# Kernel tuning notes

Hardware: AMD Instinct MI355X
Metric: run time of the kernel (lower is better)

The kernel has to match this reference:

```python
import jax, jax.numpy as jnp
import numpy as np

DIM = 512
NUM_HEADS = 8
HEAD_DIM = DIM // NUM_HEADS
B, N = 2, 4096


def setup_inputs() -> dict:
    key = jax.random.key(0)
    k1, k2, k3, k4, k5 = jax.random.split(key, 5)
    s = 1.0 / np.sqrt(DIM)
    return {
        "x": jax.random.normal(k1, (B, N, DIM), dtype=jnp.float32),
        "w_qkv": jax.random.normal(k2, (DIM, 3 * DIM), dtype=jnp.float32) * s,
        "b_qkv": jax.random.normal(k3, (3 * DIM,), dtype=jnp.float32) * 0.01,
        "w_proj": jax.random.normal(k4, (DIM, DIM), dtype=jnp.float32) * s,
        "b_proj": jax.random.normal(k5, (DIM,), dtype=jnp.float32) * 0.01,
    }


def reference(x, w_qkv, b_qkv, w_proj, b_proj):
    b, n, c = x.shape
    h, d = NUM_HEADS, HEAD_DIM
    qkv = x @ w_qkv + b_qkv                      # [B,N,3C]
    q, k, v = jnp.split(qkv, 3, axis=-1)
    # [B,N,C] -> [B,H,N,D]
    q = q.reshape(b, n, h, d).transpose(0, 2, 1, 3)
    k = k.reshape(b, n, h, d).transpose(0, 2, 1, 3)
    v = v.reshape(b, n, h, d).transpose(0, 2, 1, 3)
    scale = d ** (-0.5)
    attn = jnp.einsum('bhqd,bhkd->bhqk', q, k) * scale  # [B,H,N,N]
    attn = jax.nn.softmax(attn, axis=-1)
    out = jnp.einsum('bhqk,bhkd->bhqd', attn, v)        # [B,H,N,D]
    out = out.transpose(0, 2, 1, 3).reshape(b, n, c)
    return out @ w_proj + b_proj
```

## Files before the change

kernel.cpp:

```cpp
#include <hip/hip_runtime.h>

#define DIM_C 512
#define HEADS 8
#define HD 64
#define BATCH 2
#define SEQ 4096
#define QSCALE (0.125f * 1.44269504088896f)

typedef __attribute__((ext_vector_type(8))) short short8;
typedef __attribute__((ext_vector_type(4))) float f32x4;

__device__ __forceinline__ ushort f2bf(float f) {
    union { float f; unsigned u; } x; x.f = f;
    unsigned r = x.u + 0x7fffu + ((x.u >> 16) & 1u);
    return (ushort)(r >> 16);
}

__device__ __forceinline__ void gl_lds16(const void* g, void* l) {
    __builtin_amdgcn_global_load_lds(
        (const __attribute__((address_space(1))) unsigned int*)g,
        (__attribute__((address_space(3))) unsigned int*)l, 16, 0, 0);
}

__device__ __forceinline__ unsigned cvt_pk_bf16(float lo, float hi) {
    unsigned w;
    asm("v_cvt_pk_bf16_f32 %0, %1, %2" : "=v"(w) : "v"(lo), "v"(hi));
    return w;
}

__global__ __launch_bounds__(256)
void convert_bf16(const float* __restrict__ in, ushort* __restrict__ out, int n4) {
    int i = blockIdx.x * blockDim.x + threadIdx.x;
    const int stride = gridDim.x * blockDim.x;
    for (; i < n4; i += stride) {
        const float4 v = reinterpret_cast<const float4*>(in)[i];
        ushort4 o;
        o.x = f2bf(v.x); o.y = f2bf(v.y); o.z = f2bf(v.z); o.w = f2bf(v.w);
        reinterpret_cast<ushort4*>(out)[i] = o;
    }
}

__global__ __launch_bounds__(256)
void transpose_w_bf16(const float* __restrict__ in, ushort* __restrict__ out,
                      int R, int C) {
    __shared__ ushort Ls[64 * 68];
    const int tid = threadIdx.x;
    const int c0 = blockIdx.x * 64, r0 = blockIdx.y * 64;
    #pragma unroll
    for (int p = 0; p < 4; ++p) {
        const int idx = tid + p * 256;
        const int r = idx >> 4, c4 = (idx & 15) * 4;
        const float4 v = *reinterpret_cast<const float4*>(
            &in[(size_t)(r0 + r) * C + c0 + c4]);
        ushort4 o; o.x = f2bf(v.x); o.y = f2bf(v.y); o.z = f2bf(v.z); o.w = f2bf(v.w);
        *reinterpret_cast<ushort4*>(&Ls[r * 68 + c4]) = o;
    }
    __syncthreads();
    #pragma unroll
    for (int p = 0; p < 4; ++p) {
        const int idx = tid + p * 256;
        const int c = idx >> 4, r4 = (idx & 15) * 4;
        ushort4 o;
        o.x = Ls[(r4 + 0) * 68 + c]; o.y = Ls[(r4 + 1) * 68 + c];
        o.z = Ls[(r4 + 2) * 68 + c]; o.w = Ls[(r4 + 3) * 68 + c];
        *reinterpret_cast<ushort4*>(&out[(size_t)(c0 + c) * R + r0 + r4]) = o;
    }
}

template<int MODE>
__global__ __launch_bounds__(256)
void gemm_mfma(const ushort* __restrict__ A, const ushort* __restrict__ BT,
               const float* __restrict__ bias, void* __restrict__ Cout,
               ushort* __restrict__ vtOut, int M, int N, int K) {
    __shared__ ushort As[128 * 64];
    __shared__ ushort Bs[128 * 64];
    const int tid = threadIdx.x;
    const int lane = tid & 63, wid = tid >> 6;
    const int lr = lane & 15, lg = lane >> 4;
    const int wm = wid >> 1, wn = wid & 1;
    const int rowBase = blockIdx.y * 128, colBase = blockIdx.x * 128;
    const int l8 = lane >> 3;
    const int lchunk = (lane & 7) ^ l8;

    f32x4 acc[4][4];
    #pragma unroll
    for (int i = 0; i < 4; ++i)
        #pragma unroll
        for (int j = 0; j < 4; ++j)
            #pragma unroll
            for (int c = 0; c < 4; ++c) acc[i][j][c] = 0.f;

    for (int k0 = 0; k0 < K; k0 += 64) {
        #pragma unroll
        for (int i = 0; i < 4; ++i) {
            const int r = wid * 32 + i * 8;
            gl_lds16(&A[(size_t)(rowBase + r + l8) * K + k0 + lchunk * 8],
                     &As[r * 64]);
            gl_lds16(&BT[(size_t)(colBase + r + l8) * K + k0 + lchunk * 8],
                     &Bs[r * 64]);
        }
        __syncthreads();
        #pragma unroll
        for (int s = 0; s < 2; ++s) {
            short8 af[4], bf[4];
            #pragma unroll
            for (int mt = 0; mt < 4; ++mt) {
                const int r = wm * 64 + mt * 16 + lr;
                af[mt] = *reinterpret_cast<const short8*>(
                    &As[r * 64 + ((s * 4 + lg) ^ (r & 7)) * 8]);
            }
            #pragma unroll
            for (int nt = 0; nt < 4; ++nt) {
                const int r = wn * 64 + nt * 16 + lr;
                bf[nt] = *reinterpret_cast<const short8*>(
                    &Bs[r * 64 + ((s * 4 + lg) ^ (r & 7)) * 8]);
            }
            #pragma unroll
            for (int mt = 0; mt < 4; ++mt)
                #pragma unroll
                for (int nt = 0; nt < 4; ++nt)
                    acc[mt][nt] = __builtin_amdgcn_mfma_f32_16x16x32_bf16(
                        af[mt], bf[nt], acc[mt][nt], 0, 0, 0);
        }
        __syncthreads();
    }

    #pragma unroll
    for (int nt = 0; nt < 4; ++nt) {
        const int col = colBase + wn * 64 + nt * 16 + lr;
        const float bv = bias[col];
        if (MODE == 1 && col >= 1024) {
            const int d = col - 1024;
            const int bb = rowBase >> 12;
            const size_t vbase = ((size_t)(bb * 8 + (d >> 6)) * 64 + (d & 63)) * SEQ;
            #pragma unroll
            for (int mt = 0; mt < 4; ++mt) {
                const int n = (rowBase & (SEQ - 1)) + wm * 64 + mt * 16 + lg * 4;
                ushort4 o;
                o.x = f2bf(acc[mt][nt][0] + bv); o.y = f2bf(acc[mt][nt][1] + bv);
                o.z = f2bf(acc[mt][nt][2] + bv); o.w = f2bf(acc[mt][nt][3] + bv);
                *reinterpret_cast<ushort4*>(&vtOut[vbase + n]) = o;
            }
        } else {
            const float qs = (MODE == 1 && col < DIM_C) ? QSCALE : 1.f;
            #pragma unroll
            for (int mt = 0; mt < 4; ++mt) {
                #pragma unroll
                for (int j = 0; j < 4; ++j) {
                    const int row = rowBase + wm * 64 + mt * 16 + lg * 4 + j;
                    const float v = (acc[mt][nt][j] + bv) * qs;
                    if (MODE == 0)
                        reinterpret_cast<float*>(Cout)[(size_t)row * N + col] = v;
                    else
                        reinterpret_cast<ushort*>(Cout)[(size_t)row * N + col] = f2bf(v);
                }
            }
        }
    }
}

__global__ __launch_bounds__(512)
void flash_attn5(const ushort* __restrict__ qkvb, const ushort* __restrict__ vt,
                 ushort* __restrict__ aoutb) {
    __shared__ ushort Ks[2][64 * 64];
    __shared__ ushort Vs[2][64 * 64];
    __shared__ ushort Ps[8 * 16 * 64];

    const int tid = threadIdx.x;
    const int lane = tid & 63, wid = tid >> 6;
    const int lr = lane & 15, lg = lane >> 4;
    const int qt = blockIdx.x, bh = blockIdx.y;
    const int b = bh >> 3, h = bh & 7;
    const int q0 = qt * 128;
    const int l8 = lane >> 3;
    const int lchunk = (lane & 7) ^ l8;

    short8 qf[2];
    {
        const size_t qrow = (size_t)b * SEQ + q0 + wid * 16 + lr;
        #pragma unroll
        for (int s = 0; s < 2; ++s)
            qf[s] = *reinterpret_cast<const short8*>(
                &qkvb[qrow * 1536 + h * 64 + s * 32 + lg * 8]);
    }

    float m = -1e30f, l = 0.f;
    f32x4 oa[4];
    #pragma unroll
    for (int dt = 0; dt < 4; ++dt)
        #pragma unroll
        for (int c = 0; c < 4; ++c) oa[dt][c] = 0.f;

    auto stage = [&](int kt, int buf) {
        const int k0 = kt * 64;
        const int r = wid * 8;
        gl_lds16(&qkvb[(size_t)(b * SEQ + k0 + r + l8) * 1536 + DIM_C +
                       h * 64 + lchunk * 8],
                 &Ks[buf][r * 64]);
        gl_lds16(&vt[((size_t)bh * 64 + r + l8) * SEQ + k0 + lchunk * 8],
                 &Vs[buf][r * 64]);
    };

    stage(0, 0);
    const int NT = SEQ / 64;
    for (int kt = 0; kt < NT; ++kt) {
        const int buf = kt & 1;
        __syncthreads();
        if (kt + 1 < NT) stage(kt + 1, buf ^ 1);

        f32x4 sa[4];
        #pragma unroll
        for (int t = 0; t < 4; ++t)
            #pragma unroll
            for (int c = 0; c < 4; ++c) sa[t][c] = 0.f;
        #pragma unroll
        for (int t = 0; t < 4; ++t) {
            const int n = t * 16 + lr;
            #pragma unroll
            for (int s = 0; s < 2; ++s) {
                const short8 kf = *reinterpret_cast<const short8*>(
                    &Ks[buf][n * 64 + ((s * 4 + lg) ^ (n & 7)) * 8]);
                sa[t] = __builtin_amdgcn_mfma_f32_16x16x32_bf16(
                    kf, qf[s], sa[t], 0, 0, 0);
            }
        }

        float mx = sa[0][0];
        #pragma unroll
        for (int t = 0; t < 4; ++t)
            #pragma unroll
            for (int r = 0; r < 4; ++r) mx = fmaxf(mx, sa[t][r]);
        mx = fmaxf(mx, __shfl_xor(mx, 16));
        mx = fmaxf(mx, __shfl_xor(mx, 32));
        if (__any(mx > m + 8.f)) {
            const float mnew = fmaxf(m, mx);
            const float alpha = exp2f(m - mnew);
            m = mnew;
            l *= alpha;
            const float a0 = __shfl(alpha, lg * 4 + 0);
            const float a1 = __shfl(alpha, lg * 4 + 1);
            const float a2 = __shfl(alpha, lg * 4 + 2);
            const float a3 = __shfl(alpha, lg * 4 + 3);
            #pragma unroll
            for (int dt = 0; dt < 4; ++dt) {
                oa[dt][0] *= a0; oa[dt][1] *= a1;
                oa[dt][2] *= a2; oa[dt][3] *= a3;
            }
        }
        float sum = 0.f;
        #pragma unroll
        for (int t = 0; t < 4; ++t)
            #pragma unroll
            for (int r = 0; r < 4; ++r) {
                sa[t][r] = exp2f(sa[t][r] - m);
                sum += sa[t][r];
            }
        sum += __shfl_xor(sum, 16);
        sum += __shfl_xor(sum, 32);
        l += sum;

        const int pb = wid * (16 * 64);
        const int pbase = pb + lr * 64 + (lg & 1) * 4;
        #pragma unroll
        for (int t = 0; t < 4; ++t) {
            const int chunk = (2 * t + (lg >> 1)) ^ (lr & 7);
            uint2 w;
            w.x = cvt_pk_bf16(sa[t][0], sa[t][1]);
            w.y = cvt_pk_bf16(sa[t][2], sa[t][3]);
            *reinterpret_cast<uint2*>(&Ps[pbase + chunk * 8]) = w;
        }

        short8 pf[2];
        #pragma unroll
        for (int s = 0; s < 2; ++s)
            pf[s] = *reinterpret_cast<const short8*>(
                &Ps[pb + lr * 64 + ((lg * 8 + 32 * s) ^ ((lr & 7) << 3))]);

        #pragma unroll
        for (int dt = 0; dt < 4; ++dt) {
            const int d = dt * 16 + lr;
            #pragma unroll
            for (int s = 0; s < 2; ++s) {
                const short8 vf = *reinterpret_cast<const short8*>(
                    &Vs[buf][d * 64 + ((s * 4 + lg) ^ (d & 7)) * 8]);
                oa[dt] = __builtin_amdgcn_mfma_f32_16x16x32_bf16(
                    pf[s], vf, oa[dt], 0, 0, 0);
            }
        }
    }

    const float linv = 1.f / l;
    const float v0 = __shfl(linv, lg * 4 + 0);
    const float v1 = __shfl(linv, lg * 4 + 1);
    const float v2 = __shfl(linv, lg * 4 + 2);
    const float v3 = __shfl(linv, lg * 4 + 3);
    const size_t orow0 = (size_t)b * SEQ + q0 + wid * 16;
    #pragma unroll
    for (int dt = 0; dt < 4; ++dt) {
        const int c = h * HD + dt * 16 + lr;
        aoutb[(orow0 + lg * 4 + 0) * DIM_C + c] = f2bf(oa[dt][0] * v0);
        aoutb[(orow0 + lg * 4 + 1) * DIM_C + c] = f2bf(oa[dt][1] * v1);
        aoutb[(orow0 + lg * 4 + 2) * DIM_C + c] = f2bf(oa[dt][2] * v2);
        aoutb[(orow0 + lg * 4 + 3) * DIM_C + c] = f2bf(oa[dt][3] * v3);
    }
}

extern "C" void kernel_launch(void* const* d_in, const int* in_sizes, int n_in,
                              void* d_out, int out_size, void* d_ws, size_t ws_size,
                              hipStream_t stream) {
    const float* x      = (const float*)d_in[0];
    const float* w_qkv  = (const float*)d_in[1];
    const float* b_qkv  = (const float*)d_in[2];
    const float* w_proj = (const float*)d_in[3];
    const float* b_proj = (const float*)d_in[4];
    float* out = (float*)d_out;

    const int M = BATCH * SEQ;
    ushort* xb     = (ushort*)d_ws;
    ushort* wqkvT  = xb     + (size_t)M * DIM_C;
    ushort* wprojT = wqkvT  + (size_t)3 * DIM_C * DIM_C;
    ushort* qkvb   = wprojT + (size_t)DIM_C * DIM_C;
    ushort* vt     = qkvb   + (size_t)M * 3 * DIM_C;
    ushort* aoutb  = vt     + (size_t)16 * HD * SEQ;

    convert_bf16<<<2048, 256, 0, stream>>>(x, xb, M * DIM_C / 4);
    transpose_w_bf16<<<dim3(3 * DIM_C / 64, DIM_C / 64), 256, 0, stream>>>(
        w_qkv, wqkvT, DIM_C, 3 * DIM_C);
    transpose_w_bf16<<<dim3(DIM_C / 64, DIM_C / 64), 256, 0, stream>>>(
        w_proj, wprojT, DIM_C, DIM_C);

    gemm_mfma<1><<<dim3(3 * DIM_C / 128, M / 128), 256, 0, stream>>>(
        xb, wqkvT, b_qkv, qkvb, vt, M, 3 * DIM_C, DIM_C);

    flash_attn5<<<dim3(SEQ / 128, BATCH * HEADS), 512, 0, stream>>>(
        qkvb, vt, aoutb);

    gemm_mfma<0><<<dim3(DIM_C / 128, M / 128), 256, 0, stream>>>(
        aoutb, wprojT, b_proj, out, nullptr, M, DIM_C, DIM_C);
}
```

Measured before the change: 256.1 us.

## Vectorize GEMM epilogue, split V transpose, add setprio and new P swizzle

Swaps the MFMA operand order in the GEMM so each lane holds four consecutive columns. This lets the epilogue write float4/uint2 vectors with a vectorized bias load instead of scalar strided stores. The transposed V write is moved out of the QKV GEMM into a separate LDS transpose kernel, which adds a launch and an extra pass over V. The attention kernel also raises wave priority around its MFMA blocks and changes the P-buffer LDS swizzle to reduce bank conflicts.

```diff
diff --git a/kernel.cpp b/kernel.cpp
--- a/kernel.cpp
+++ b/kernel.cpp
@@ -67,11 +67,37 @@
     }
 }
 
+__global__ __launch_bounds__(256)
+void transpose_v(const ushort* __restrict__ qkvb, ushort* __restrict__ vt) {
+    __shared__ ushort Ls[64 * 68];
+    const int tid = threadIdx.x;
+    const int n0 = blockIdx.x * 64;
+    const int bh = blockIdx.y, b = bh >> 3, h = bh & 7;
+    #pragma unroll
+    for (int p = 0; p < 4; ++p) {
+        const int idx = tid + p * 256;
+        const int r = idx >> 4, c4 = (idx & 15) * 4;
+        const ushort4 v = *reinterpret_cast<const ushort4*>(
+            &qkvb[(size_t)(b * SEQ + n0 + r) * 1536 + 1024 + h * 64 + c4]);
+        *reinterpret_cast<ushort4*>(&Ls[r * 68 + c4]) = v;
+    }
+    __syncthreads();
+    #pragma unroll
+    for (int p = 0; p < 4; ++p) {
+        const int idx = tid + p * 256;
+        const int d = idx >> 4, n4 = (idx & 15) * 4;
+        ushort4 o;
+        o.x = Ls[(n4 + 0) * 68 + d]; o.y = Ls[(n4 + 1) * 68 + d];
+        o.z = Ls[(n4 + 2) * 68 + d]; o.w = Ls[(n4 + 3) * 68 + d];
+        *reinterpret_cast<ushort4*>(&vt[((size_t)bh * 64 + d) * SEQ + n0 + n4]) = o;
+    }
+}
+
 template<int MODE>
 __global__ __launch_bounds__(256)
 void gemm_mfma(const ushort* __restrict__ A, const ushort* __restrict__ BT,
                const float* __restrict__ bias, void* __restrict__ Cout,
-               ushort* __restrict__ vtOut, int M, int N, int K) {
+               int M, int N, int K) {
     __shared__ ushort As[128 * 64];
     __shared__ ushort Bs[128 * 64];
     const int tid = threadIdx.x;
@@ -120,40 +146,33 @@
                 #pragma unroll
                 for (int nt = 0; nt < 4; ++nt)
                     acc[mt][nt] = __builtin_amdgcn_mfma_f32_16x16x32_bf16(
-                        af[mt], bf[nt], acc[mt][nt], 0, 0, 0);
+                        bf[nt], af[mt], acc[mt][nt], 0, 0, 0);
         }
         __syncthreads();
     }
 
     #pragma unroll
     for (int nt = 0; nt < 4; ++nt) {
-        const int col = colBase + wn * 64 + nt * 16 + lr;
-        const float bv = bias[col];
-        if (MODE == 1 && col >= 1024) {
-            const int d = col - 1024;
-            const int bb = rowBase >> 12;
-            const size_t vbase = ((size_t)(bb * 8 + (d >> 6)) * 64 + (d & 63)) * SEQ;
-            #pragma unroll
-            for (int mt = 0; mt < 4; ++mt) {
-                const int n = (rowBase & (SEQ - 1)) + wm * 64 + mt * 16 + lg * 4;
-                ushort4 o;
-                o.x = f2bf(acc[mt][nt][0] + bv); o.y = f2bf(acc[mt][nt][1] + bv);
-                o.z = f2bf(acc[mt][nt][2] + bv); o.w = f2bf(acc[mt][nt][3] + bv);
-                *reinterpret_cast<ushort4*>(&vtOut[vbase + n]) = o;
-            }
-        } else {
-            const float qs = (MODE == 1 && col < DIM_C) ? QSCALE : 1.f;
-            #pragma unroll
-            for (int mt = 0; mt < 4; ++mt) {
-                #pragma unroll
-                for (int j = 0; j < 4; ++j) {
-                    const int row = rowBase + wm * 64 + mt * 16 + lg * 4 + j;
-                    const float v = (acc[mt][nt][j] + bv) * qs;
-                    if (MODE == 0)
-                        reinterpret_cast<float*>(Cout)[(size_t)row * N + col] = v;
-                    else
-                        reinterpret_cast<ushort*>(Cout)[(size_t)row * N + col] = f2bf(v);
-                }
+        const int c0 = colBase + wn * 64 + nt * 16 + lg * 4;
+        const float4 bv = *reinterpret_cast<const float4*>(&bias[c0]);
+        const float qs = (MODE == 1 && c0 < DIM_C) ? QSCALE : 1.f;
+        #pragma unroll
+        for (int mt = 0; mt < 4; ++mt) {
+            const int row = rowBase + wm * 64 + mt * 16 + lr;
+            if (MODE == 0) {
+                float4 o;
+                o.x = acc[mt][nt][0] + bv.x; o.y = acc[mt][nt][1] + bv.y;
+                o.z = acc[mt][nt][2] + bv.z; o.w = acc[mt][nt][3] + bv.w;
+                *reinterpret_cast<float4*>(
+                    &reinterpret_cast<float*>(Cout)[(size_t)row * N + c0]) = o;
+            } else {
+                uint2 o;
+                o.x = cvt_pk_bf16((acc[mt][nt][0] + bv.x) * qs,
+                                  (acc[mt][nt][1] + bv.y) * qs);
+                o.y = cvt_pk_bf16((acc[mt][nt][2] + bv.z) * qs,
+                                  (acc[mt][nt][3] + bv.w) * qs);
+                *reinterpret_cast<uint2*>(
+                    &reinterpret_cast<ushort*>(Cout)[(size_t)row * N + c0]) = o;
             }
         }
     }
@@ -174,6 +193,7 @@
     const int q0 = qt * 128;
     const int l8 = lane >> 3;
     const int lchunk = (lane & 7) ^ l8;
+    const int rsw = (lr & 7) ^ ((lr >> 3) << 2);
 
     short8 qf[2];
     {
@@ -213,6 +233,7 @@
         for (int t = 0; t < 4; ++t)
             #pragma unroll
             for (int c = 0; c < 4; ++c) sa[t][c] = 0.f;
+        __builtin_amdgcn_s_setprio(1);
         #pragma unroll
         for (int t = 0; t < 4; ++t) {
             const int n = t * 16 + lr;
@@ -224,6 +245,7 @@
                     kf, qf[s], sa[t], 0, 0, 0);
             }
         }
+        __builtin_amdgcn_s_setprio(0);
 
         float mx = sa[0][0];
         #pragma unroll
@@ -263,7 +285,7 @@
         const int pbase = pb + lr * 64 + (lg & 1) * 4;
         #pragma unroll
         for (int t = 0; t < 4; ++t) {
-            const int chunk = (2 * t + (lg >> 1)) ^ (lr & 7);
+            const int chunk = (2 * t + (lg >> 1)) ^ rsw;
             uint2 w;
             w.x = cvt_pk_bf16(sa[t][0], sa[t][1]);
             w.y = cvt_pk_bf16(sa[t][2], sa[t][3]);
@@ -274,8 +296,9 @@
         #pragma unroll
         for (int s = 0; s < 2; ++s)
             pf[s] = *reinterpret_cast<const short8*>(
-                &Ps[pb + lr * 64 + ((lg * 8 + 32 * s) ^ ((lr & 7) << 3))]);
-
+                &Ps[pb + lr * 64 + ((lg + 4 * s) ^ rsw) * 8]);
+
+        __builtin_amdgcn_s_setprio(1);
         #pragma unroll
         for (int dt = 0; dt < 4; ++dt) {
             const int d = dt * 16 + lr;
@@ -287,6 +310,7 @@
                     pf[s], vf, oa[dt], 0, 0, 0);
             }
         }
+        __builtin_amdgcn_s_setprio(0);
     }
 
     const float linv = 1.f / l;
@@ -330,11 +354,13 @@
         w_proj, wprojT, DIM_C, DIM_C);
 
     gemm_mfma<1><<<dim3(3 * DIM_C / 128, M / 128), 256, 0, stream>>>(
-        xb, wqkvT, b_qkv, qkvb, vt, M, 3 * DIM_C, DIM_C);
+        xb, wqkvT, b_qkv, qkvb, M, 3 * DIM_C, DIM_C);
+
+    transpose_v<<<dim3(SEQ / 64, BATCH * HEADS), 256, 0, stream>>>(qkvb, vt);
 
     flash_attn5<<<dim3(SEQ / 128, BATCH * HEADS), 512, 0, stream>>>(
         qkvb, vt, aoutb);
 
     gemm_mfma<0><<<dim3(DIM_C / 128, M / 128), 256, 0, stream>>>(
-        aoutb, wprojT, b_proj, out, nullptr, M, DIM_C, DIM_C);
-}
+        aoutb, wprojT, b_proj, out, M, DIM_C, DIM_C);
+}
```

Result: no change. 254.9 us (-0.5%).
